# Performance work log

Hardware: AMD Instinct MI355X
Metric: run time of the kernel (lower is better)

## Reference

```python
import jax, jax.numpy as jnp
import numpy as np

NEG_INF = -9e15  # matches torch's -9000000000000000.0 mask value
LEAKY_SLOPE = 0.2  # init alpha


def setup_inputs() -> dict:
    key = jax.random.key(0)
    k1, k2, k3, k4 = jax.random.split(key, 4)
    N, dim = 4096, 128
    hidden = jax.random.normal(k1, (N, dim), dtype=jnp.float32)
    adj = jax.random.randint(k2, (N, N), 0, 5)  # relation codes 0..4
    W = jax.random.normal(k3, (4, dim), dtype=jnp.float32) * (1.0 / np.sqrt(dim))
    b = jax.random.normal(k4, (4,), dtype=jnp.float32) * 0.01
    return {"hidden": hidden, "adj": adj, "W": W, "b": b}


def reference(hidden, adj, W, b):
    # e_k[i,j] = leakyrelu(sum_d h[i,d]*h[j,d]*W[k,d] + b[k])
    # equivalent to the torch repeat/view outer-product + four dim->1 Linears,
    # computed without materializing the [N,N,dim] intermediate.
    hw = hidden[None, :, :] * W[:, None, :]               # [4, N, dim]
    e = jnp.einsum('knd,md->knm', hw, hidden) + b[:, None, None]  # [4, N, N]
    e = jax.nn.leaky_relu(e, negative_slope=LEAKY_SLOPE)
    neg = jnp.asarray(NEG_INF, dtype=e.dtype)
    alpha = jnp.where(adj == 1, e[0], neg)
    alpha = jnp.where(adj == 2, e[1], alpha)
    alpha = jnp.where(adj == 3, e[2], alpha)
    alpha = jnp.where(adj == 4, e[3], alpha)
    alpha = jax.nn.softmax(alpha, axis=-1)                # [N, N]
    return alpha @ hidden                                  # [N, dim]
```

## Files before the change

### kernel.cpp

```cpp
#include <hip/hip_runtime.h>

#define NN 4096
#define DIM 128
#define TN 32
#define TM 64
#define NTILES 16
#define NSPLIT 4

typedef __attribute__((ext_vector_type(8))) short bf16x8;
typedef __attribute__((ext_vector_type(4))) float f32x4;

#define LSTRIDE 136
#define HCST    72
#define HROW_USH (TM * LSTRIDE)
#define HCOL_USH (DIM * HCST)
#define TILE_USH (HROW_USH + HCOL_USH)
#define TILE_CHUNKS 35
#define PST 72

__device__ inline unsigned short f2bf(float x) {
    union { float f; unsigned u; } v; v.f = x;
    unsigned r = v.u + 0x7FFFu + ((v.u >> 16) & 1u);
    return (unsigned short)(r >> 16);
}

__device__ inline void dma16(const void* g, void* l) {
    __builtin_amdgcn_global_load_lds(
        (const __attribute__((address_space(1))) void*)g,
        (__attribute__((address_space(3))) void*)l,
        16, 0, 0);
}

__global__ __launch_bounds__(256) void prep_pack_kernel(
    const float* __restrict__ hidden,
    unsigned short* __restrict__ Hpack)
{
    __shared__ unsigned short T[DIM * HCST];
    const int tid = threadIdx.x;
    const int t0  = blockIdx.x;
    const int m0  = t0 * TM;
    unsigned short* rowdst = Hpack + (size_t)t0 * TILE_USH;
    unsigned short* coldst = rowdst + HROW_USH;

    #pragma unroll
    for (int it = 0; it < 8; ++it) {
        int idx = tid + 256 * it;
        int row = idx >> 5;
        int c4  = (idx & 31) * 4;
        float4 v = *(const float4*)(hidden + (size_t)(m0 + row) * DIM + c4);
        ushort4 o;
        o.x = f2bf(v.x); o.y = f2bf(v.y); o.z = f2bf(v.z); o.w = f2bf(v.w);
        *(ushort4*)(rowdst + row * LSTRIDE + c4) = o;
        T[(c4 + 0) * HCST + row] = o.x;
        T[(c4 + 1) * HCST + row] = o.y;
        T[(c4 + 2) * HCST + row] = o.z;
        T[(c4 + 3) * HCST + row] = o.w;
    }
    __syncthreads();
    #pragma unroll
    for (int it = 0; it < 4; ++it) {
        int idx = tid + 256 * it;
        int d  = idx >> 3;
        int c8 = (idx & 7) * 8;
        uint4 v = *(const uint4*)(T + d * HCST + c8);
        *(uint4*)(coldst + d * HCST + c8) = v;
    }
}

__global__ __launch_bounds__(512, 4) void gat_flash_kernel(
    const float* __restrict__ hidden,
    const unsigned short* __restrict__ Hpack,
    const int*   __restrict__ adj,
    const float* __restrict__ W,
    const float* __restrict__ bvec,
    float*       __restrict__ Opart,
    float*       __restrict__ lpart)
{
    __shared__ __align__(16) unsigned short HH[2][TILE_USH];
    __shared__ __align__(16) unsigned short Plc[TN * PST];
    __shared__ float redsum[8][16];

    const int tid  = threadIdx.x;
    const int w    = tid >> 6;
    const int lane = tid & 63;
    const int g    = lane >> 4;
    const int l15  = lane & 15;
    const int blk  = blockIdx.x;
    const int nb   = blk >> 2;
    const int qtr  = blk & 3;
    const int n0   = nb * TN;
    const int gt0  = qtr * NTILES;
    const int rg   = w >> 2;
    const int ms   = w & 3;
    const int lofs = lane * 16;
    const float NEG = -9.0e15f;

    const float b0 = bvec[0], b1 = bvec[1], b2 = bvec[2], b3 = bvec[3];

    {
        const char* src = (const char*)(Hpack + (size_t)gt0 * TILE_USH);
        char* dst = (char*)&HH[0][0];
        #pragma unroll
        for (int it = 0; it < 5; ++it) {
            int chunk = it * 8 + w;
            if (chunk < TILE_CHUNKS)
                dma16(src + chunk * 1024 + lofs, dst + chunk * 1024);
        }
    }
    {
        int qr = tid >> 2;
        int r  = qr & 31;
        int d0 = (tid & 3) * 32;
        const float* hrow = hidden + (size_t)(n0 + r) * DIM + d0;
        const float* wrow = W + (qr >> 5) * DIM + d0;
        unsigned short* qdst = &HH[1][qr * LSTRIDE + d0];
        #pragma unroll
        for (int c = 0; c < 8; ++c) {
            float4 hv = *(const float4*)(hrow + 4 * c);
            float4 wv = *(const float4*)(wrow + 4 * c);
            ushort4 o;
            o.x = f2bf(hv.x * wv.x); o.y = f2bf(hv.y * wv.y);
            o.z = f2bf(hv.z * wv.z); o.w = f2bf(hv.w * wv.w);
            *(ushort4*)(qdst + 4 * c) = o;
        }
    }
    __syncthreads();

    bf16x8 Af[4][4];
    #pragma unroll
    for (int k = 0; k < 4; ++k)
        #pragma unroll
        for (int ks = 0; ks < 4; ++ks)
            Af[k][ks] = *(const bf16x8*)&HH[1][(k * 32 + rg * 16 + l15) * LSTRIDE + ks * 32 + 8 * g];
    __syncthreads();

    float lrow[4] = {0.f, 0.f, 0.f, 0.f};
    f32x4 Oacc[2];
    Oacc[0] = (f32x4){0.f, 0.f, 0.f, 0.f};
    Oacc[1] = (f32x4){0.f, 0.f, 0.f, 0.f};

    int avc[4], avn[4];
    #pragma unroll
    for (int t = 0; t < 4; ++t)
        avc[t] = adj[(size_t)(n0 + rg * 16 + 4 * g + t) * NN + gt0 * TM + ms * 16 + l15];

    for (int tile = 0; tile < NTILES; ++tile) {
        const int cur = tile & 1;
        const int nxt = cur ^ 1;

        if (tile + 1 < NTILES) {
            const char* src = (const char*)(Hpack + (size_t)(gt0 + tile + 1) * TILE_USH);
            char* dst = (char*)&HH[nxt][0];
            #pragma unroll
            for (int it = 0; it < 5; ++it) {
                int chunk = it * 8 + w;
                if (chunk < TILE_CHUNKS)
                    dma16(src + chunk * 1024 + lofs, dst + chunk * 1024);
            }
            #pragma unroll
            for (int t = 0; t < 4; ++t)
                avn[t] = adj[(size_t)(n0 + rg * 16 + 4 * g + t) * NN + (gt0 + tile + 1) * TM + ms * 16 + l15];
        }

        f32x4 S[4];
        #pragma unroll
        for (int k = 0; k < 4; ++k) S[k] = (f32x4){0.f, 0.f, 0.f, 0.f};
        #pragma unroll
        for (int ks = 0; ks < 4; ++ks) {
            bf16x8 B = *(const bf16x8*)&HH[cur][(ms * 16 + l15) * LSTRIDE + ks * 32 + 8 * g];
            #pragma unroll
            for (int k = 0; k < 4; ++k)
                S[k] = __builtin_amdgcn_mfma_f32_16x16x32_bf16(Af[k][ks], B, S[k], 0, 0, 0);
        }

        #pragma unroll
        for (int t = 0; t < 4; ++t) {
            int a = avc[t];
            float s = S[0][t] + b0;
            s = (a == 2) ? S[1][t] + b1 : s;
            s = (a == 3) ? S[2][t] + b2 : s;
            s = (a == 4) ? S[3][t] + b3 : s;
            float e = fmaxf(s, 0.2f * s);
            e = (a == 0) ? NEG : e;
            float p = __expf(e);
            lrow[t] += p;
            Plc[(rg * 16 + 4 * g + t) * PST + ms * 16 + l15] = f2bf(p);
        }

        asm volatile("s_waitcnt lgkmcnt(0)\n\ts_barrier" ::: "memory");

        #pragma unroll
        for (int c4 = 0; c4 < 2; ++c4) {
            bf16x8 Pa = *(const bf16x8*)&Plc[(rg * 16 + l15) * PST + c4 * 32 + 8 * g];
            #pragma unroll
            for (int dt = 0; dt < 2; ++dt) {
                bf16x8 Bv = *(const bf16x8*)&HH[cur][HROW_USH + (ms * 32 + dt * 16 + l15) * HCST + c4 * 32 + 8 * g];
                Oacc[dt] = __builtin_amdgcn_mfma_f32_16x16x32_bf16(Pa, Bv, Oacc[dt], 0, 0, 0);
            }
        }

        #pragma unroll
        for (int t = 0; t < 4; ++t) avc[t] = avn[t];
        __syncthreads();
    }

    #pragma unroll
    for (int t = 0; t < 4; ++t) {
        float v = lrow[t];
        v += __shfl_xor(v, 1); v += __shfl_xor(v, 2);
        v += __shfl_xor(v, 4); v += __shfl_xor(v, 8);
        if (l15 == 0) redsum[w][4 * g + t] = v;
    }
    __syncthreads();
    if (tid < 32) {
        int rgp = tid >> 4, rr = tid & 15;
        float s = redsum[rgp * 4 + 0][rr] + redsum[rgp * 4 + 1][rr]
                + redsum[rgp * 4 + 2][rr] + redsum[rgp * 4 + 3][rr];
        lpart[blk * 32 + tid] = s;
    }
    float* Ob = Opart + (size_t)blk * TN * DIM;
    #pragma unroll
    for (int dt = 0; dt < 2; ++dt)
        #pragma unroll
        for (int t = 0; t < 4; ++t)
            Ob[(rg * 16 + 4 * g + t) * DIM + ms * 32 + dt * 16 + l15] = Oacc[dt][t];
}

__global__ __launch_bounds__(256) void combine_kernel(
    const float* __restrict__ Opart, const float* __restrict__ lpart,
    float* __restrict__ out)
{
    int idx = blockIdx.x * 256 + threadIdx.x;
    int r = idx >> 7, d = idx & 127;
    int nb = r >> 5, rr = r & 31;
    float O = 0.f, l = 0.f;
    #pragma unroll
    for (int q = 0; q < NSPLIT; ++q) {
        O += Opart[(size_t)(nb * NSPLIT + q) * (TN * DIM) + rr * 128 + d];
        l += lpart[(nb * NSPLIT + q) * 32 + rr];
    }
    out[idx] = O / l;
}

extern "C" void kernel_launch(void* const* d_in, const int* in_sizes, int n_in,
                              void* d_out, int out_size, void* d_ws, size_t ws_size,
                              hipStream_t stream) {
    const float* hidden = (const float*)d_in[0];
    const int*   adj    = (const int*)d_in[1];
    const float* W      = (const float*)d_in[2];
    const float* b      = (const float*)d_in[3];
    float* out = (float*)d_out;

    char* ws = (char*)d_ws;
    unsigned short* Hpack = (unsigned short*)ws;
    float* Opart = (float*)(ws + (4u << 20));
    float* lpart = (float*)(ws + (12u << 20));

    prep_pack_kernel<<<NN / TM, 256, 0, stream>>>(hidden, Hpack);
    gat_flash_kernel<<<512, 512, 0, stream>>>(hidden, Hpack, adj, W, b, Opart, lpart);
    combine_kernel<<<NN * DIM / 256, 256, 0, stream>>>(Opart, lpart, out);
}
```

Before: 149.5 us.

## Double query rows per block, split keys eight ways, per-wave P staging

```diff
diff --git a/kernel.cpp b/kernel.cpp
--- a/kernel.cpp
+++ b/kernel.cpp
@@ -2,10 +2,10 @@
 
 #define NN 4096
 #define DIM 128
-#define TN 32
+#define TN 64
 #define TM 64
-#define NTILES 16
-#define NSPLIT 4
+#define NSPLIT 8
+#define NTILES 8
 
 typedef __attribute__((ext_vector_type(8))) short bf16x8;
 typedef __attribute__((ext_vector_type(4))) float f32x4;
@@ -16,7 +16,8 @@
 #define HCOL_USH (DIM * HCST)
 #define TILE_USH (HROW_USH + HCOL_USH)
 #define TILE_CHUNKS 35
-#define PST 72
+#define PWST 36
+#define PW_USH (16 * PWST)
 
 __device__ inline unsigned short f2bf(float x) {
     union { float f; unsigned u; } v; v.f = x;
@@ -77,7 +78,7 @@
     float*       __restrict__ lpart)
 {
     __shared__ __align__(16) unsigned short HH[2][TILE_USH];
-    __shared__ __align__(16) unsigned short Plc[TN * PST];
+    __shared__ __align__(16) unsigned short Plc[8 * PW_USH];
     __shared__ float redsum[8][16];
 
     const int tid  = threadIdx.x;
@@ -86,12 +87,12 @@
     const int g    = lane >> 4;
     const int l15  = lane & 15;
     const int blk  = blockIdx.x;
-    const int nb   = blk >> 2;
-    const int qtr  = blk & 3;
-    const int n0   = nb * TN;
-    const int gt0  = qtr * NTILES;
-    const int rg   = w >> 2;
-    const int ms   = w & 3;
+    const int nbr  = blk >> 3;
+    const int q8   = blk & 7;
+    const int n0   = nbr * TN;
+    const int gt0  = q8 * NTILES;
+    const int rg   = w >> 1;
+    const int ms   = w & 1;
     const int lofs = lane * 16;
     const float NEG = -9.0e15f;
 
@@ -107,42 +108,54 @@
                 dma16(src + chunk * 1024 + lofs, dst + chunk * 1024);
         }
     }
+    bf16x8 Af[4][4];
     {
-        int qr = tid >> 2;
-        int r  = qr & 31;
-        int d0 = (tid & 3) * 32;
-        const float* hrow = hidden + (size_t)(n0 + r) * DIM + d0;
-        const float* wrow = W + (qr >> 5) * DIM + d0;
-        unsigned short* qdst = &HH[1][qr * LSTRIDE + d0];
-        #pragma unroll
-        for (int c = 0; c < 8; ++c) {
-            float4 hv = *(const float4*)(hrow + 4 * c);
-            float4 wv = *(const float4*)(wrow + 4 * c);
-            ushort4 o;
-            o.x = f2bf(hv.x * wv.x); o.y = f2bf(hv.y * wv.y);
-            o.z = f2bf(hv.z * wv.z); o.w = f2bf(hv.w * wv.w);
-            *(ushort4*)(qdst + 4 * c) = o;
-        }
-    }
+        const float* hr = hidden + (size_t)(n0 + rg * 16 + l15) * DIM;
+        float4 hv[4][2];
+        #pragma unroll
+        for (int ks = 0; ks < 4; ++ks) {
+            hv[ks][0] = *(const float4*)(hr + ks * 32 + 8 * g);
+            hv[ks][1] = *(const float4*)(hr + ks * 32 + 8 * g + 4);
+        }
+        #pragma unroll
+        for (int k = 0; k < 4; ++k) {
+            const float* wr = W + k * DIM;
+            #pragma unroll
+            for (int ks = 0; ks < 4; ++ks) {
+                float4 w0 = *(const float4*)(wr + ks * 32 + 8 * g);
+                float4 w1 = *(const float4*)(wr + ks * 32 + 8 * g + 4);
+                union { unsigned short u[8]; bf16x8 v; } c;
+                c.u[0] = f2bf(hv[ks][0].x * w0.x);
+                c.u[1] = f2bf(hv[ks][0].y * w0.y);
+                c.u[2] = f2bf(hv[ks][0].z * w0.z);
+                c.u[3] = f2bf(hv[ks][0].w * w0.w);
+                c.u[4] = f2bf(hv[ks][1].x * w1.x);
+                c.u[5] = f2bf(hv[ks][1].y * w1.y);
+                c.u[6] = f2bf(hv[ks][1].z * w1.z);
+                c.u[7] = f2bf(hv[ks][1].w * w1.w);
+                Af[k][ks] = c.v;
+            }
+        }
+    }
+
+    float lrow[4] = {0.f, 0.f, 0.f, 0.f};
+    f32x4 Oacc[8];
+    #pragma unroll
+    for (int dt = 0; dt < 8; ++dt) Oacc[dt] = (f32x4){0.f, 0.f, 0.f, 0.f};
+
+    int avc[8], avn[8];
+    #pragma unroll
+    for (int i = 0; i < 8; ++i) avn[i] = 0;
+    #pragma unroll
+    for (int ch = 0; ch < 2; ++ch)
+        #pragma unroll
+        for (int t = 0; t < 4; ++t)
+            avc[ch * 4 + t] = adj[(size_t)(n0 + rg * 16 + 4 * g + t) * NN
+                                  + gt0 * TM + ms * 32 + ch * 16 + l15];
+
     __syncthreads();
 
-    bf16x8 Af[4][4];
-    #pragma unroll
-    for (int k = 0; k < 4; ++k)
-        #pragma unroll
-        for (int ks = 0; ks < 4; ++ks)
-            Af[k][ks] = *(const bf16x8*)&HH[1][(k * 32 + rg * 16 + l15) * LSTRIDE + ks * 32 + 8 * g];
-    __syncthreads();
-
-    float lrow[4] = {0.f, 0.f, 0.f, 0.f};
-    f32x4 Oacc[2];
-    Oacc[0] = (f32x4){0.f, 0.f, 0.f, 0.f};
-    Oacc[1] = (f32x4){0.f, 0.f, 0.f, 0.f};
-
-    int avc[4], avn[4];
-    #pragma unroll
-    for (int t = 0; t < 4; ++t)
-        avc[t] = adj[(size_t)(n0 + rg * 16 + 4 * g + t) * NN + gt0 * TM + ms * 16 + l15];
+    unsigned short* Pw = &Plc[w * PW_USH];
 
     for (int tile = 0; tile < NTILES; ++tile) {
         const int cur = tile & 1;
@@ -158,49 +171,63 @@
                     dma16(src + chunk * 1024 + lofs, dst + chunk * 1024);
             }
             #pragma unroll
-            for (int t = 0; t < 4; ++t)
-                avn[t] = adj[(size_t)(n0 + rg * 16 + 4 * g + t) * NN + (gt0 + tile + 1) * TM + ms * 16 + l15];
-        }
-
-        f32x4 S[4];
-        #pragma unroll
-        for (int k = 0; k < 4; ++k) S[k] = (f32x4){0.f, 0.f, 0.f, 0.f};
+            for (int ch = 0; ch < 2; ++ch)
+                #pragma unroll
+                for (int t = 0; t < 4; ++t)
+                    avn[ch * 4 + t] = adj[(size_t)(n0 + rg * 16 + 4 * g + t) * NN
+                                          + (gt0 + tile + 1) * TM + ms * 32 + ch * 16 + l15];
+        }
+
+        f32x4 S[4][2];
+        #pragma unroll
+        for (int k = 0; k < 4; ++k) {
+            S[k][0] = (f32x4){0.f, 0.f, 0.f, 0.f};
+            S[k][1] = (f32x4){0.f, 0.f, 0.f, 0.f};
+        }
         #pragma unroll
         for (int ks = 0; ks < 4; ++ks) {
-            bf16x8 B = *(const bf16x8*)&HH[cur][(ms * 16 + l15) * LSTRIDE + ks * 32 + 8 * g];
-            #pragma unroll
-            for (int k = 0; k < 4; ++k)
-                S[k] = __builtin_amdgcn_mfma_f32_16x16x32_bf16(Af[k][ks], B, S[k], 0, 0, 0);
-        }
-
-        #pragma unroll
-        for (int t = 0; t < 4; ++t) {
-            int a = avc[t];
-            float s = S[0][t] + b0;
-            s = (a == 2) ? S[1][t] + b1 : s;
-            s = (a == 3) ? S[2][t] + b2 : s;
-            s = (a == 4) ? S[3][t] + b3 : s;
-            float e = fmaxf(s, 0.2f * s);
-            e = (a == 0) ? NEG : e;
-            float p = __expf(e);
-            lrow[t] += p;
-            Plc[(rg * 16 + 4 * g + t) * PST + ms * 16 + l15] = f2bf(p);
-        }
-
-        asm volatile("s_waitcnt lgkmcnt(0)\n\ts_barrier" ::: "memory");
-
-        #pragma unroll
-        for (int c4 = 0; c4 < 2; ++c4) {
-            bf16x8 Pa = *(const bf16x8*)&Plc[(rg * 16 + l15) * PST + c4 * 32 + 8 * g];
-            #pragma unroll
-            for (int dt = 0; dt < 2; ++dt) {
-                bf16x8 Bv = *(const bf16x8*)&HH[cur][HROW_USH + (ms * 32 + dt * 16 + l15) * HCST + c4 * 32 + 8 * g];
-                Oacc[dt] = __builtin_amdgcn_mfma_f32_16x16x32_bf16(Pa, Bv, Oacc[dt], 0, 0, 0);
-            }
-        }
-
-        #pragma unroll
-        for (int t = 0; t < 4; ++t) avc[t] = avn[t];
+            #pragma unroll
+            for (int ch = 0; ch < 2; ++ch) {
+                bf16x8 B = *(const bf16x8*)&HH[cur][(ms * 32 + ch * 16 + l15) * LSTRIDE + ks * 32 + 8 * g];
+                #pragma unroll
+                for (int k = 0; k < 4; ++k)
+                    S[k][ch] = __builtin_amdgcn_mfma_f32_16x16x32_bf16(Af[k][ks], B, S[k][ch], 0, 0, 0);
+            }
+        }
+
+        #pragma unroll
+        for (int ch = 0; ch < 2; ++ch) {
+            #pragma unroll
+            for (int t = 0; t < 4; ++t) {
+                int a = avc[ch * 4 + t];
+                float s = S[0][ch][t] + b0;
+                s = (a == 2) ? S[1][ch][t] + b1 : s;
+                s = (a == 3) ? S[2][ch][t] + b2 : s;
+                s = (a == 4) ? S[3][ch][t] + b3 : s;
+                float e = fmaxf(s, 0.2f * s);
+                e = (a == 0) ? NEG : e;
+                float p = __expf(e);
+                lrow[t] += p;
+                Pw[(4 * g + t) * PWST + ch * 16 + l15] = f2bf(p);
+            }
+        }
+
+        union { uint2 u2[2]; bf16x8 v; } pc;
+        {
+            const uint2* pp = (const uint2*)&Pw[l15 * PWST + 8 * g];
+            pc.u2[0] = pp[0];
+            pc.u2[1] = pp[1];
+        }
+        bf16x8 Pa = pc.v;
+
+        #pragma unroll
+        for (int dt = 0; dt < 8; ++dt) {
+            bf16x8 Bv = *(const bf16x8*)&HH[cur][HROW_USH + (dt * 16 + l15) * HCST + ms * 32 + 8 * g];
+            Oacc[dt] = __builtin_amdgcn_mfma_f32_16x16x32_bf16(Pa, Bv, Oacc[dt], 0, 0, 0);
+        }
+
+        #pragma unroll
+        for (int i = 0; i < 8; ++i) avc[i] = avn[i];
         __syncthreads();
     }
 
@@ -211,19 +238,29 @@
         v += __shfl_xor(v, 4); v += __shfl_xor(v, 8);
         if (l15 == 0) redsum[w][4 * g + t] = v;
     }
+    float* HHf = (float*)&HH[0][0];
+    #pragma unroll
+    for (int dt = 0; dt < 8; ++dt)
+        #pragma unroll
+        for (int t = 0; t < 4; ++t)
+            HHf[w * 2048 + (4 * g + t) * 128 + dt * 16 + l15] = Oacc[dt][t];
     __syncthreads();
-    if (tid < 32) {
-        int rgp = tid >> 4, rr = tid & 15;
-        float s = redsum[rgp * 4 + 0][rr] + redsum[rgp * 4 + 1][rr]
-                + redsum[rgp * 4 + 2][rr] + redsum[rgp * 4 + 3][rr];
-        lpart[blk * 32 + tid] = s;
-    }
-    float* Ob = Opart + (size_t)blk * TN * DIM;
-    #pragma unroll
-    for (int dt = 0; dt < 2; ++dt)
-        #pragma unroll
-        for (int t = 0; t < 4; ++t)
-            Ob[(rg * 16 + 4 * g + t) * DIM + ms * 32 + dt * 16 + l15] = Oacc[dt][t];
+    {
+        float* Ob = Opart + (size_t)blk * (TN * DIM);
+        #pragma unroll
+        for (int i = 0; i < 16; ++i) {
+            int e = tid + 512 * i;
+            int r = e >> 7, d = e & 127;
+            int rg2 = r >> 4, rr = r & 15;
+            float s = HHf[(rg2 * 2 + 0) * 2048 + rr * 128 + d]
+                    + HHf[(rg2 * 2 + 1) * 2048 + rr * 128 + d];
+            Ob[e] = s;
+        }
+        if (tid < TN) {
+            int rg2 = tid >> 4, rr = tid & 15;
+            lpart[blk * TN + tid] = redsum[rg2 * 2 + 0][rr] + redsum[rg2 * 2 + 1][rr];
+        }
+    }
 }
 
 __global__ __launch_bounds__(256) void combine_kernel(
@@ -232,12 +269,12 @@
 {
     int idx = blockIdx.x * 256 + threadIdx.x;
     int r = idx >> 7, d = idx & 127;
-    int nb = r >> 5, rr = r & 31;
+    int nbr = r >> 6, rr = r & 63;
     float O = 0.f, l = 0.f;
     #pragma unroll
     for (int q = 0; q < NSPLIT; ++q) {
-        O += Opart[(size_t)(nb * NSPLIT + q) * (TN * DIM) + rr * 128 + d];
-        l += lpart[(nb * NSPLIT + q) * 32 + rr];
+        O += Opart[(size_t)(nbr * NSPLIT + q) * (TN * DIM) + rr * 128 + d];
+        l += lpart[(nbr * NSPLIT + q) * TN + rr];
     }
     out[idx] = O / l;
 }
@@ -254,7 +291,7 @@
     char* ws = (char*)d_ws;
     unsigned short* Hpack = (unsigned short*)ws;
     float* Opart = (float*)(ws + (4u << 20));
-    float* lpart = (float*)(ws + (12u << 20));
+    float* lpart = (float*)(ws + (20u << 20));
 
     prep_pack_kernel<<<NN / TM, 256, 0, stream>>>(hidden, Hpack);
     gat_flash_kernel<<<512, 512, 0, stream>>>(hidden, Hpack, adj, W, b, Opart, lpart);
```

New measurement: 235.8 us. 1.58x slower.
